# Performance work log

Measured on AMD Instinct MI355X. Metric: run time of the kernel, lower is better.

The kernel has to match this reference:

```python
import jax, jax.numpy as jnp
import numpy as np

DIM = 1024
NUM_HEADS = 16
HEAD_DIM = DIM // NUM_HEADS


def setup_inputs() -> dict:
    key = jax.random.key(0)
    ks = jax.random.split(key, 5)
    B, T = 2, 2048
    x = jax.random.normal(ks[0], (B, T, DIM), dtype=jnp.float32)
    s = 1.0 / np.sqrt(DIM)
    # weights stored [in, out] so y = x @ W + b (equivalent to torch Linear)
    W_qkv = jax.random.uniform(ks[1], (DIM, 3 * DIM), jnp.float32, -s, s)
    b_qkv = jax.random.uniform(ks[2], (3 * DIM,), jnp.float32, -s, s)
    W_proj = jax.random.uniform(ks[3], (DIM, DIM), jnp.float32, -s, s)
    b_proj = jax.random.uniform(ks[4], (DIM,), jnp.float32, -s, s)
    return {"x": x, "W_qkv": W_qkv, "b_qkv": b_qkv, "W_proj": W_proj, "b_proj": b_proj}


def reference(x, W_qkv, b_qkv, W_proj, b_proj):
    B, T, C = x.shape
    H, D = NUM_HEADS, HEAD_DIM
    qkv = x @ W_qkv + b_qkv                       # [B, T, 3C]
    qkv = qkv.reshape(B, T, 3, H, D)
    q = jnp.transpose(qkv[:, :, 0], (0, 2, 1, 3))  # [B, H, T, D]
    k = jnp.transpose(qkv[:, :, 1], (0, 2, 1, 3))
    v = jnp.transpose(qkv[:, :, 2], (0, 2, 1, 3))
    scale = 1.0 / np.sqrt(D).astype(np.float32)
    attn = jnp.einsum('bhqd,bhkd->bhqk', q, k) * scale  # [B, H, T, T]
    causal = jnp.tril(jnp.ones((T, T), dtype=bool))
    attn = jnp.where(causal, attn, -jnp.inf)
    attn = jax.nn.softmax(attn, axis=-1)
    out = jnp.einsum('bhqk,bhkd->bhqd', attn, v)        # [B, H, T, D]
    out = jnp.transpose(out, (0, 2, 1, 3)).reshape(B, T, C)
    return out @ W_proj + b_proj
```

## Files before the change

kernel.cpp:

```cpp
#include <hip/hip_runtime.h>
#include <hip/hip_bf16.h>
#include <cstddef>
#include <cstdint>

#define DIM   1024
#define NH    16
#define HD    64
#define BATCH 2
#define SEQ   2048
#define NROWS (BATCH * SEQ)
#define QSCALE 0.1803368801111204f

typedef __bf16 bfrag  __attribute__((ext_vector_type(8)));
typedef float  f32x4  __attribute__((ext_vector_type(4)));

#if __has_builtin(__builtin_amdgcn_exp2f)
#define EXP2F(x) __builtin_amdgcn_exp2f(x)
#else
#define EXP2F(x) exp2f(x)
#endif

__device__ __forceinline__ unsigned short f2bf(float f) {
  union { float f; uint32_t u; } v; v.f = f;
  uint32_t r = (v.u + 0x7FFF + ((v.u >> 16) & 1)) >> 16;
  return (unsigned short)r;
}

__device__ __forceinline__ void async_copy16(const unsigned short* g,
                                             unsigned short* l) {
  __builtin_amdgcn_global_load_lds(
      (const __attribute__((address_space(1))) unsigned int*)g,
      (__attribute__((address_space(3))) unsigned int*)l, 16, 0, 0);
}

__global__ __launch_bounds__(256) void cvt_x(const float* __restrict__ x,
                                             unsigned short* __restrict__ xb) {
  int i = (blockIdx.x * 256 + threadIdx.x) * 4;
  float4 v = *(const float4*)(x + i);
  ushort4 p = {f2bf(v.x), f2bf(v.y), f2bf(v.z), f2bf(v.w)};
  *(ushort4*)(xb + i) = p;
}

__global__ __launch_bounds__(256) void cvt_t(const float* __restrict__ src,
                                             unsigned short* __restrict__ dst,
                                             int R, int C) {
  __shared__ float t[32][33];
  const int r0 = blockIdx.y * 32, c0 = blockIdx.x * 32;
  const int tx = threadIdx.x, ty = threadIdx.y;
#pragma unroll
  for (int i = 0; i < 4; ++i)
    t[ty + i * 8][tx] = src[(size_t)(r0 + ty + i * 8) * C + c0 + tx];
  __syncthreads();
#pragma unroll
  for (int i = 0; i < 4; ++i)
    dst[(size_t)(c0 + ty + i * 8) * R + r0 + tx] = f2bf(t[tx][ty + i * 8]);
}

__global__ __launch_bounds__(256) void qkv_mfma(
    const unsigned short* __restrict__ Ax,
    const unsigned short* __restrict__ Bt,
    const float* __restrict__ bias,
    unsigned short* __restrict__ Qb, unsigned short* __restrict__ Kf,
    unsigned short* __restrict__ Vf) {
  const int row0 = blockIdx.y * 128;
  const int col0 = blockIdx.x * 128;
  const int tid  = threadIdx.x;
  const int lane = tid & 63;
  const int wave = tid >> 6;
  const int col  = lane & 15;
  const int quad = lane >> 4;
  const int wm = wave >> 1, wn = wave & 1;

  __shared__ unsigned short As[128 * 32];
  __shared__ unsigned short Bs[128 * 32];

  const int which = col0 >> 10;

  f32x4 acc[4][4];
#pragma unroll
  for (int i = 0; i < 4; ++i)
#pragma unroll
    for (int j = 0; j < 4; ++j) acc[i][j] = (f32x4){0.f, 0.f, 0.f, 0.f};

  if (which == 2) {
    for (int k0 = 0; k0 < DIM; k0 += 32) {
      __syncthreads();
#pragma unroll
      for (int it = 0; it < 2; ++it) {
        int c = tid + it * 256;
        int r = c >> 2, o8 = (c & 3) * 8;
        async_copy16(Ax + (size_t)(row0 + r) * DIM + k0 + o8, &As[c * 8]);
        async_copy16(Bt + (size_t)(col0 + r) * DIM + k0 + o8, &Bs[c * 8]);
      }
      __syncthreads();
      bfrag a[4], b[4];
#pragma unroll
      for (int i = 0; i < 4; ++i)
        a[i] = *(const bfrag*)&As[(wm * 64 + i * 16 + col) * 32 + quad * 8];
#pragma unroll
      for (int j = 0; j < 4; ++j)
        b[j] = *(const bfrag*)&Bs[(wn * 64 + j * 16 + col) * 32 + quad * 8];
#pragma unroll
      for (int i = 0; i < 4; ++i)
#pragma unroll
        for (int j = 0; j < 4; ++j)
          acc[i][j] = __builtin_amdgcn_mfma_f32_16x16x32_bf16(
              a[i], b[j], acc[i][j], 0, 0, 0);
    }
  } else {
    for (int k0 = 0; k0 < DIM; k0 += 32) {
      __syncthreads();
#pragma unroll
      for (int it = 0; it < 2; ++it) {
        int c = tid + it * 256;
        int r = c >> 2, o8 = (c & 3) * 8;
        async_copy16(Ax + (size_t)(row0 + r) * DIM + k0 + o8, &As[c * 8]);
        async_copy16(Bt + (size_t)(col0 + r) * DIM + k0 + o8, &Bs[c * 8]);
      }
      __syncthreads();
      bfrag a[4], b[4];
#pragma unroll
      for (int i = 0; i < 4; ++i)
        a[i] = *(const bfrag*)&As[(wm * 64 + i * 16 + col) * 32 + quad * 8];
#pragma unroll
      for (int j = 0; j < 4; ++j)
        b[j] = *(const bfrag*)&Bs[(wn * 64 + j * 16 + col) * 32 + quad * 8];
#pragma unroll
      for (int i = 0; i < 4; ++i)
#pragma unroll
        for (int j = 0; j < 4; ++j)
          acc[i][j] = __builtin_amdgcn_mfma_f32_16x16x32_bf16(
              b[j], a[i], acc[i][j], 0, 0, 0);
    }
  }

  const int bb = row0 >> 11;
  const int hq = ((col0 + wn * 64) & 1023) >> 6;
  const int bh = bb * NH + hq;
  const int t  = ((row0 + wm * 64) & 2047) >> 6;

  if (which == 2) {
    float bj[4];
#pragma unroll
    for (int j = 0; j < 4; ++j) bj[j] = bias[col0 + wn * 64 + j * 16 + col];
#pragma unroll
    for (int i = 0; i < 4; ++i) {
      const size_t base_i =
          (((size_t)bh * 32 + t) * 8) * 512 + (size_t)((i >> 1) & 1) * 512 +
          (size_t)(quad & 1) * 4;
      const int rowsub = (i * 2 + (quad >> 1)) & 3;
#pragma unroll
      for (int j = 0; j < 4; ++j) {
        ushort4 pk = {f2bf(acc[i][j][0] + bj[j]), f2bf(acc[i][j][1] + bj[j]),
                      f2bf(acc[i][j][2] + bj[j]), f2bf(acc[i][j][3] + bj[j])};
        const size_t idx =
            base_i + (size_t)j * 1024 + (size_t)(rowsub * 16 + col) * 8;
        *(ushort4*)&Vf[idx] = pk;
      }
    }
  } else {
    const int ttl = row0 + wm * 64;
#pragma unroll
    for (int j = 0; j < 4; ++j) {
      const float4 b4 =
          *(const float4*)&bias[col0 + wn * 64 + j * 16 + quad * 4];
#pragma unroll
      for (int i = 0; i < 4; ++i) {
        f32x4 v = acc[i][j];
        v[0] += b4.x; v[1] += b4.y; v[2] += b4.z; v[3] += b4.w;
        if (which == 0) {
          v[0] *= QSCALE; v[1] *= QSCALE; v[2] *= QSCALE; v[3] *= QSCALE;
          ushort4 pk = {f2bf(v[0]), f2bf(v[1]), f2bf(v[2]), f2bf(v[3])};
          const int tt = (ttl + i * 16 + col) & 2047;
          *(ushort4*)&Qb[((size_t)bh * SEQ + tt) * HD + j * 16 + quad * 4] = pk;
        } else {
          ushort4 pk = {f2bf(v[0]), f2bf(v[1]), f2bf(v[2]), f2bf(v[3])};
          const int kg = ((col >> 2) & 1) | ((i >> 1) << 1);
          const int ck = ((i * 2 + (col >> 3)) & 3) * 4 + (col & 3);
          const size_t idx =
              ((((size_t)bh * 32 + t) * 4 + kg) * 2 + (j >> 1)) * 512 +
              (size_t)(((j & 1) * 2 + (quad >> 1)) * 16 + ck) * 8 +
              (quad & 1) * 4;
          *(ushort4*)&Kf[idx] = pk;
        }
      }
    }
  }
}

__global__ __launch_bounds__(256) void flash_mfma(
    const unsigned short* __restrict__ Qb, const unsigned short* __restrict__ Kf,
    const unsigned short* __restrict__ Vf, unsigned short* __restrict__ Abf) {
  const int blk  = blockIdx.x;
  const int bh   = blk & 31;
  const int qc   = 63 - (blk >> 5);
  const int q0   = qc * 32;
  const int tid  = threadIdx.x;
  const int lane = tid & 63;
  const int wave = tid >> 6;
  const int col  = lane & 15;
  const int quad = lane >> 4;

  const int ntiles = (qc >> 1) + 1;
  const int nw     = (ntiles < 4) ? ntiles : 4;

  __shared__ float Om[4][64][33];
  __shared__ float Ml[4][4][32];

  bfrag qb[2][2];
  {
    const unsigned short* qp = Qb + ((size_t)bh * SEQ + q0 + col) * HD;
    qb[0][0] = *(const bfrag*)(qp + quad * 8);
    qb[0][1] = *(const bfrag*)(qp + 32 + quad * 8);
    qb[1][0] = *(const bfrag*)(qp + 16 * HD + quad * 8);
    qb[1][1] = *(const bfrag*)(qp + 16 * HD + 32 + quad * 8);
  }

  const unsigned short* kfb = Kf + (size_t)bh * SEQ * HD + lane * 8;
  const unsigned short* vfb = Vf + (size_t)bh * SEQ * HD + lane * 8;

  f32x4 o[2][4];
#pragma unroll
  for (int qf = 0; qf < 2; ++qf)
#pragma unroll
    for (int n = 0; n < 4; ++n) o[qf][n] = (f32x4){0.f, 0.f, 0.f, 0.f};
  float l_p[2] = {0.f, 0.f};

  auto loadK = [&](int t, bfrag (&kd)[4][2]) {
    const unsigned short* p = kfb + (size_t)t * 4096;
#pragma unroll
    for (int kg = 0; kg < 4; ++kg) {
      kd[kg][0] = *(const bfrag*)(p + (kg * 2 + 0) * 512);
      kd[kg][1] = *(const bfrag*)(p + (kg * 2 + 1) * 512);
    }
  };

  auto proc = [&](int t, bfrag (&kc)[4][2], bfrag (&kn)[4][2]) {
    const int k0 = t * 64;
    bfrag va[4][2];
    {
      const unsigned short* p = vfb + (size_t)t * 4096;
#pragma unroll
      for (int n = 0; n < 4; ++n) {
        va[n][0] = *(const bfrag*)(p + (n * 2 + 0) * 512);
        va[n][1] = *(const bfrag*)(p + (n * 2 + 1) * 512);
      }
    }
    loadK((t + 4 < ntiles) ? t + 4 : t, kn);

    const bool last = (t == ntiles - 1);
#pragma unroll
    for (int qf = 0; qf < 2; ++qf) {
      f32x4 s[4];
#pragma unroll
      for (int kg = 0; kg < 4; ++kg) {
        f32x4 c = (f32x4){0.f, 0.f, 0.f, 0.f};
        c = __builtin_amdgcn_mfma_f32_16x16x32_bf16(kc[kg][0], qb[qf][0], c,
                                                    0, 0, 0);
        c = __builtin_amdgcn_mfma_f32_16x16x32_bf16(kc[kg][1], qb[qf][1], c,
                                                    0, 0, 0);
        s[kg] = c;
      }
      if (last) {
        const int q = q0 + qf * 16 + col;
#pragma unroll
        for (int kg = 0; kg < 4; ++kg)
#pragma unroll
          for (int r = 0; r < 4; ++r) {
            int key = k0 + quad * 8 + (kg & 1) * 4 + r + (kg & 2) * 16;
            if (key > q) s[kg][r] = -3.0e38f;
          }
      }
      float lsum = 0.f;
#pragma unroll
      for (int kg = 0; kg < 4; ++kg)
#pragma unroll
        for (int r = 0; r < 4; ++r) {
          float p = EXP2F(s[kg][r]);
          s[kg][r] = p;
          lsum += p;
        }
      l_p[qf] += lsum;

      bfrag pa0, pa1;
#pragma unroll
      for (int r = 0; r < 4; ++r) {
        pa0[r]     = (__bf16)s[0][r];
        pa0[4 + r] = (__bf16)s[1][r];
        pa1[r]     = (__bf16)s[2][r];
        pa1[4 + r] = (__bf16)s[3][r];
      }
#pragma unroll
      for (int n = 0; n < 4; ++n) {
        o[qf][n] = __builtin_amdgcn_mfma_f32_16x16x32_bf16(va[n][0], pa0,
                                                           o[qf][n], 0, 0, 0);
        o[qf][n] = __builtin_amdgcn_mfma_f32_16x16x32_bf16(va[n][1], pa1,
                                                           o[qf][n], 0, 0, 0);
      }
    }
  };

  if (wave < ntiles) {
    bfrag kaA[4][2], kaB[4][2];
    loadK(wave, kaA);
    for (int t = wave; t < ntiles; t += 8) {
      proc(t, kaA, kaB);
      if (t + 4 < ntiles) proc(t + 4, kaB, kaA);
    }
  }

  if (wave < nw) {
#pragma unroll
    for (int qf = 0; qf < 2; ++qf)
#pragma unroll
      for (int n = 0; n < 4; ++n)
#pragma unroll
        for (int r = 0; r < 4; ++r)
          Om[wave][n * 16 + quad * 4 + r][qf * 16 + col] = o[qf][n][r];
#pragma unroll
    for (int qf = 0; qf < 2; ++qf)
      Ml[wave][quad][qf * 16 + col] = l_p[qf];
  }
  __syncthreads();

  {
    const int q  = tid & 31;
    const int d0 = (tid >> 5) * 8;
    float lt = 0.f;
    for (int w = 0; w < nw; ++w)
#pragma unroll
      for (int qd = 0; qd < 4; ++qd) lt += Ml[w][qd][q];
    float acc[8] = {};
    for (int w = 0; w < nw; ++w)
#pragma unroll
      for (int j = 0; j < 8; ++j) acc[j] += Om[w][d0 + j][q];
    const float inv = 1.0f / lt;
    const int b = bh >> 4, h = bh & 15;
    unsigned short* dst = Abf + ((size_t)b * SEQ + q0 + q) * DIM + h * HD + d0;
    ushort4 p1 = {f2bf(acc[0] * inv), f2bf(acc[1] * inv),
                  f2bf(acc[2] * inv), f2bf(acc[3] * inv)};
    ushort4 p2 = {f2bf(acc[4] * inv), f2bf(acc[5] * inv),
                  f2bf(acc[6] * inv), f2bf(acc[7] * inv)};
    *(ushort4*)dst = p1;
    *(ushort4*)(dst + 4) = p2;
  }
}

__global__ __launch_bounds__(256) void proj_mfma(
    const unsigned short* __restrict__ Ax,
    const unsigned short* __restrict__ Bt,
    const float* __restrict__ bias, float* __restrict__ out) {
  const int row0 = blockIdx.y * 128;
  const int col0 = blockIdx.x * 128;
  const int tid  = threadIdx.x;
  const int lane = tid & 63;
  const int wave = tid >> 6;
  const int col  = lane & 15;
  const int quad = lane >> 4;
  const int wm = wave >> 1, wn = wave & 1;

  __shared__ unsigned short As[128 * 32];
  __shared__ unsigned short Bs[128 * 32];

  f32x4 acc[4][4];
#pragma unroll
  for (int i = 0; i < 4; ++i)
#pragma unroll
    for (int j = 0; j < 4; ++j) acc[i][j] = (f32x4){0.f, 0.f, 0.f, 0.f};

  for (int k0 = 0; k0 < DIM; k0 += 32) {
    __syncthreads();
#pragma unroll
    for (int it = 0; it < 2; ++it) {
      int c = tid + it * 256;
      int r = c >> 2, o8 = (c & 3) * 8;
      async_copy16(Ax + (size_t)(row0 + r) * DIM + k0 + o8, &As[c * 8]);
      async_copy16(Bt + (size_t)(col0 + r) * DIM + k0 + o8, &Bs[c * 8]);
    }
    __syncthreads();

    bfrag a[4], b[4];
#pragma unroll
    for (int i = 0; i < 4; ++i)
      a[i] = *(const bfrag*)&As[(wm * 64 + i * 16 + col) * 32 + quad * 8];
#pragma unroll
    for (int j = 0; j < 4; ++j)
      b[j] = *(const bfrag*)&Bs[(wn * 64 + j * 16 + col) * 32 + quad * 8];
#pragma unroll
    for (int i = 0; i < 4; ++i)
#pragma unroll
      for (int j = 0; j < 4; ++j)
        acc[i][j] = __builtin_amdgcn_mfma_f32_16x16x32_bf16(
            b[j], a[i], acc[i][j], 0, 0, 0);
  }

#pragma unroll
  for (int j = 0; j < 4; ++j) {
    const int c4 = col0 + wn * 64 + j * 16 + quad * 4;
    const float4 b4 = *(const float4*)&bias[c4];
#pragma unroll
    for (int i = 0; i < 4; ++i) {
      const int tt = row0 + wm * 64 + i * 16 + col;
      float4 v = {acc[i][j][0] + b4.x, acc[i][j][1] + b4.y,
                  acc[i][j][2] + b4.z, acc[i][j][3] + b4.w};
      *(float4*)&out[(size_t)tt * DIM + c4] = v;
    }
  }
}

extern "C" void kernel_launch(void* const* d_in, const int* in_sizes, int n_in,
                              void* d_out, int out_size, void* d_ws, size_t ws_size,
                              hipStream_t stream) {
  const float* x      = (const float*)d_in[0];
  const float* W_qkv  = (const float*)d_in[1];
  const float* b_qkv  = (const float*)d_in[2];
  const float* W_proj = (const float*)d_in[3];
  const float* b_proj = (const float*)d_in[4];
  float* out = (float*)d_out;

  const size_t qkv_elems = (size_t)BATCH * NH * SEQ * HD;
  unsigned short* Qb  = (unsigned short*)d_ws;
  unsigned short* Kf  = Qb + qkv_elems;
  unsigned short* Vf  = Kf + qkv_elems;
  unsigned short* Abf = Vf + qkv_elems;
  unsigned short* xb  = Abf + qkv_elems;
  unsigned short* Wtq = xb + (size_t)NROWS * DIM;
  unsigned short* Wtp = Wtq + (size_t)3072 * DIM;

  cvt_x<<<dim3(NROWS * DIM / 1024), 256, 0, stream>>>(x, xb);
  cvt_t<<<dim3(3072 / 32, DIM / 32), dim3(32, 8), 0, stream>>>(W_qkv, Wtq,
                                                               DIM, 3072);
  cvt_t<<<dim3(DIM / 32, DIM / 32), dim3(32, 8), 0, stream>>>(W_proj, Wtp,
                                                              DIM, DIM);

  qkv_mfma<<<dim3(3072 / 128, NROWS / 128), 256, 0, stream>>>(
      xb, Wtq, b_qkv, Qb, Kf, Vf);

  flash_mfma<<<dim3(BATCH * NH * (SEQ / 32)), 256, 0, stream>>>(Qb, Kf, Vf,
                                                                Abf);

  proj_mfma<<<dim3(DIM / 128, NROWS / 128), 256, 0, stream>>>(
      Abf, Wtp, b_proj, out);
}
```

Measured before the change: 177.7 us.

## Fuse conversion kernels, deepen GEMM K-tile to 64, shrink proj N-tile

Merges the three fp32-to-bf16 conversion and transpose kernels into one launch using block-index ranges, which saves launch overhead. The QKV and projection GEMMs now load 64-wide K slices per iteration, halving the number of barrier pairs and doubling the work done between syncs. The projection GEMM switches to a 128x64 tile with each wave owning 32 rows, which doubles its grid from 256 to 512 blocks to fill more CUs. In exchange, shared memory per block rises and the projection loses some operand reuse per block.

```diff
diff --git a/kernel.cpp b/kernel.cpp
--- a/kernel.cpp
+++ b/kernel.cpp
@@ -33,20 +33,34 @@
       (__attribute__((address_space(3))) unsigned int*)l, 16, 0, 0);
 }
 
-__global__ __launch_bounds__(256) void cvt_x(const float* __restrict__ x,
-                                             unsigned short* __restrict__ xb) {
-  int i = (blockIdx.x * 256 + threadIdx.x) * 4;
-  float4 v = *(const float4*)(x + i);
-  ushort4 p = {f2bf(v.x), f2bf(v.y), f2bf(v.z), f2bf(v.w)};
-  *(ushort4*)(xb + i) = p;
-}
-
-__global__ __launch_bounds__(256) void cvt_t(const float* __restrict__ src,
-                                             unsigned short* __restrict__ dst,
-                                             int R, int C) {
+__global__ __launch_bounds__(256) void cvt_all(
+    const float* __restrict__ x, unsigned short* __restrict__ xb,
+    const float* __restrict__ Wq, unsigned short* __restrict__ Wtq,
+    const float* __restrict__ Wp, unsigned short* __restrict__ Wtp) {
+  int bid = blockIdx.x;
+  const int tid = threadIdx.x;
+  if (bid < 4096) {
+    int i = (bid * 256 + tid) * 4;
+    float4 v = *(const float4*)(x + i);
+    ushort4 p = {f2bf(v.x), f2bf(v.y), f2bf(v.z), f2bf(v.w)};
+    *(ushort4*)(xb + i) = p;
+    return;
+  }
+  bid -= 4096;
+  const float* src;
+  unsigned short* dst;
+  int R, C, bx, by;
+  if (bid < 3072) {
+    src = Wq; dst = Wtq; R = DIM; C = 3072;
+    bx = bid % 96; by = bid / 96;
+  } else {
+    bid -= 3072;
+    src = Wp; dst = Wtp; R = DIM; C = DIM;
+    bx = bid & 31; by = bid >> 5;
+  }
   __shared__ float t[32][33];
-  const int r0 = blockIdx.y * 32, c0 = blockIdx.x * 32;
-  const int tx = threadIdx.x, ty = threadIdx.y;
+  const int r0 = by * 32, c0 = bx * 32;
+  const int tx = tid & 31, ty = tid >> 5;
 #pragma unroll
   for (int i = 0; i < 4; ++i)
     t[ty + i * 8][tx] = src[(size_t)(r0 + ty + i * 8) * C + c0 + tx];
@@ -71,8 +85,8 @@
   const int quad = lane >> 4;
   const int wm = wave >> 1, wn = wave & 1;
 
-  __shared__ unsigned short As[128 * 32];
-  __shared__ unsigned short Bs[128 * 32];
+  __shared__ unsigned short As[128 * 64];
+  __shared__ unsigned short Bs[128 * 64];
 
   const int which = col0 >> 10;
 
@@ -83,54 +97,64 @@
     for (int j = 0; j < 4; ++j) acc[i][j] = (f32x4){0.f, 0.f, 0.f, 0.f};
 
   if (which == 2) {
-    for (int k0 = 0; k0 < DIM; k0 += 32) {
+    for (int k0 = 0; k0 < DIM; k0 += 64) {
       __syncthreads();
 #pragma unroll
-      for (int it = 0; it < 2; ++it) {
+      for (int it = 0; it < 4; ++it) {
         int c = tid + it * 256;
-        int r = c >> 2, o8 = (c & 3) * 8;
+        int r = c >> 3, o8 = (c & 7) * 8;
         async_copy16(Ax + (size_t)(row0 + r) * DIM + k0 + o8, &As[c * 8]);
         async_copy16(Bt + (size_t)(col0 + r) * DIM + k0 + o8, &Bs[c * 8]);
       }
       __syncthreads();
-      bfrag a[4], b[4];
-#pragma unroll
-      for (int i = 0; i < 4; ++i)
-        a[i] = *(const bfrag*)&As[(wm * 64 + i * 16 + col) * 32 + quad * 8];
-#pragma unroll
-      for (int j = 0; j < 4; ++j)
-        b[j] = *(const bfrag*)&Bs[(wn * 64 + j * 16 + col) * 32 + quad * 8];
-#pragma unroll
-      for (int i = 0; i < 4; ++i)
+#pragma unroll
+      for (int ks = 0; ks < 2; ++ks) {
+        bfrag a[4], b[4];
+#pragma unroll
+        for (int i = 0; i < 4; ++i)
+          a[i] = *(const bfrag*)&As[(wm * 64 + i * 16 + col) * 64 + ks * 32 +
+                                    quad * 8];
 #pragma unroll
         for (int j = 0; j < 4; ++j)
-          acc[i][j] = __builtin_amdgcn_mfma_f32_16x16x32_bf16(
-              a[i], b[j], acc[i][j], 0, 0, 0);
+          b[j] = *(const bfrag*)&Bs[(wn * 64 + j * 16 + col) * 64 + ks * 32 +
+                                    quad * 8];
+#pragma unroll
+        for (int i = 0; i < 4; ++i)
+#pragma unroll
+          for (int j = 0; j < 4; ++j)
+            acc[i][j] = __builtin_amdgcn_mfma_f32_16x16x32_bf16(
+                a[i], b[j], acc[i][j], 0, 0, 0);
+      }
     }
   } else {
-    for (int k0 = 0; k0 < DIM; k0 += 32) {
+    for (int k0 = 0; k0 < DIM; k0 += 64) {
       __syncthreads();
 #pragma unroll
-      for (int it = 0; it < 2; ++it) {
+      for (int it = 0; it < 4; ++it) {
         int c = tid + it * 256;
-        int r = c >> 2, o8 = (c & 3) * 8;
+        int r = c >> 3, o8 = (c & 7) * 8;
         async_copy16(Ax + (size_t)(row0 + r) * DIM + k0 + o8, &As[c * 8]);
         async_copy16(Bt + (size_t)(col0 + r) * DIM + k0 + o8, &Bs[c * 8]);
       }
       __syncthreads();
-      bfrag a[4], b[4];
-#pragma unroll
-      for (int i = 0; i < 4; ++i)
-        a[i] = *(const bfrag*)&As[(wm * 64 + i * 16 + col) * 32 + quad * 8];
-#pragma unroll
-      for (int j = 0; j < 4; ++j)
-        b[j] = *(const bfrag*)&Bs[(wn * 64 + j * 16 + col) * 32 + quad * 8];
-#pragma unroll
-      for (int i = 0; i < 4; ++i)
+#pragma unroll
+      for (int ks = 0; ks < 2; ++ks) {
+        bfrag a[4], b[4];
+#pragma unroll
+        for (int i = 0; i < 4; ++i)
+          a[i] = *(const bfrag*)&As[(wm * 64 + i * 16 + col) * 64 + ks * 32 +
+                                    quad * 8];
 #pragma unroll
         for (int j = 0; j < 4; ++j)
-          acc[i][j] = __builtin_amdgcn_mfma_f32_16x16x32_bf16(
-              b[j], a[i], acc[i][j], 0, 0, 0);
+          b[j] = *(const bfrag*)&Bs[(wn * 64 + j * 16 + col) * 64 + ks * 32 +
+                                    quad * 8];
+#pragma unroll
+        for (int i = 0; i < 4; ++i)
+#pragma unroll
+          for (int j = 0; j < 4; ++j)
+            acc[i][j] = __builtin_amdgcn_mfma_f32_16x16x32_bf16(
+                b[j], a[i], acc[i][j], 0, 0, 0);
+      }
     }
   }
 
@@ -351,56 +375,64 @@
     const unsigned short* __restrict__ Bt,
     const float* __restrict__ bias, float* __restrict__ out) {
   const int row0 = blockIdx.y * 128;
-  const int col0 = blockIdx.x * 128;
+  const int col0 = blockIdx.x * 64;
   const int tid  = threadIdx.x;
   const int lane = tid & 63;
   const int wave = tid >> 6;
   const int col  = lane & 15;
   const int quad = lane >> 4;
-  const int wm = wave >> 1, wn = wave & 1;
-
-  __shared__ unsigned short As[128 * 32];
-  __shared__ unsigned short Bs[128 * 32];
-
-  f32x4 acc[4][4];
-#pragma unroll
-  for (int i = 0; i < 4; ++i)
+
+  __shared__ unsigned short As[128 * 64];
+  __shared__ unsigned short Bs[64 * 64];
+
+  f32x4 acc[2][4];
+#pragma unroll
+  for (int i = 0; i < 2; ++i)
 #pragma unroll
     for (int j = 0; j < 4; ++j) acc[i][j] = (f32x4){0.f, 0.f, 0.f, 0.f};
 
-  for (int k0 = 0; k0 < DIM; k0 += 32) {
+  for (int k0 = 0; k0 < DIM; k0 += 64) {
     __syncthreads();
+#pragma unroll
+    for (int it = 0; it < 4; ++it) {
+      int c = tid + it * 256;
+      int r = c >> 3, o8 = (c & 7) * 8;
+      async_copy16(Ax + (size_t)(row0 + r) * DIM + k0 + o8, &As[c * 8]);
+    }
 #pragma unroll
     for (int it = 0; it < 2; ++it) {
       int c = tid + it * 256;
-      int r = c >> 2, o8 = (c & 3) * 8;
-      async_copy16(Ax + (size_t)(row0 + r) * DIM + k0 + o8, &As[c * 8]);
+      int r = c >> 3, o8 = (c & 7) * 8;
       async_copy16(Bt + (size_t)(col0 + r) * DIM + k0 + o8, &Bs[c * 8]);
     }
     __syncthreads();
 
-    bfrag a[4], b[4];
-#pragma unroll
-    for (int i = 0; i < 4; ++i)
-      a[i] = *(const bfrag*)&As[(wm * 64 + i * 16 + col) * 32 + quad * 8];
-#pragma unroll
-    for (int j = 0; j < 4; ++j)
-      b[j] = *(const bfrag*)&Bs[(wn * 64 + j * 16 + col) * 32 + quad * 8];
-#pragma unroll
-    for (int i = 0; i < 4; ++i)
+#pragma unroll
+    for (int ks = 0; ks < 2; ++ks) {
+      bfrag a[2], b[4];
+#pragma unroll
+      for (int i = 0; i < 2; ++i)
+        a[i] = *(const bfrag*)&As[(wave * 32 + i * 16 + col) * 64 + ks * 32 +
+                                  quad * 8];
 #pragma unroll
       for (int j = 0; j < 4; ++j)
-        acc[i][j] = __builtin_amdgcn_mfma_f32_16x16x32_bf16(
-            b[j], a[i], acc[i][j], 0, 0, 0);
+        b[j] = *(const bfrag*)&Bs[(j * 16 + col) * 64 + ks * 32 + quad * 8];
+#pragma unroll
+      for (int i = 0; i < 2; ++i)
+#pragma unroll
+        for (int j = 0; j < 4; ++j)
+          acc[i][j] = __builtin_amdgcn_mfma_f32_16x16x32_bf16(
+              b[j], a[i], acc[i][j], 0, 0, 0);
+    }
   }
 
 #pragma unroll
   for (int j = 0; j < 4; ++j) {
-    const int c4 = col0 + wn * 64 + j * 16 + quad * 4;
+    const int c4 = col0 + j * 16 + quad * 4;
     const float4 b4 = *(const float4*)&bias[c4];
 #pragma unroll
-    for (int i = 0; i < 4; ++i) {
-      const int tt = row0 + wm * 64 + i * 16 + col;
+    for (int i = 0; i < 2; ++i) {
+      const int tt = row0 + wave * 32 + i * 16 + col;
       float4 v = {acc[i][j][0] + b4.x, acc[i][j][1] + b4.y,
                   acc[i][j][2] + b4.z, acc[i][j][3] + b4.w};
       *(float4*)&out[(size_t)tt * DIM + c4] = v;
@@ -427,11 +459,8 @@
   unsigned short* Wtq = xb + (size_t)NROWS * DIM;
   unsigned short* Wtp = Wtq + (size_t)3072 * DIM;
 
-  cvt_x<<<dim3(NROWS * DIM / 1024), 256, 0, stream>>>(x, xb);
-  cvt_t<<<dim3(3072 / 32, DIM / 32), dim3(32, 8), 0, stream>>>(W_qkv, Wtq,
-                                                               DIM, 3072);
-  cvt_t<<<dim3(DIM / 32, DIM / 32), dim3(32, 8), 0, stream>>>(W_proj, Wtp,
-                                                              DIM, DIM);
+  cvt_all<<<dim3(4096 + 3072 + 1024), 256, 0, stream>>>(x, xb, W_qkv, Wtq,
+                                                        W_proj, Wtp);
 
   qkv_mfma<<<dim3(3072 / 128, NROWS / 128), 256, 0, stream>>>(
       xb, Wtq, b_qkv, Qb, Kf, Vf);
@@ -439,6 +468,6 @@
   flash_mfma<<<dim3(BATCH * NH * (SEQ / 32)), 256, 0, stream>>>(Qb, Kf, Vf,
                                                                 Abf);
 
-  proj_mfma<<<dim3(DIM / 128, NROWS / 128), 256, 0, stream>>>(
+  proj_mfma<<<dim3(DIM / 64, NROWS / 128), 256, 0, stream>>>(
       Abf, Wtp, b_proj, out);
 }
```

Measured after the change: 188.6 us. 6.1% more time.
